# Kernel optimization log

Hardware: AMD Instinct MI355X
Metric: run time of the kernel (lower is better)

Reference implementation:

```python
import math
import jax, jax.numpy as jnp
import numpy as np

B, C, NH, H, W = 8, 512, 4, 64, 64
CH = C // 8          # qkv channels = 64
HC = CH // NH        # head channels = 16


def _pos_encoding(c, h, w):
    # Faithful to torch code, including the raw memory reinterpretation of
    # pos_h (h, c) -> (1, c, h, 1) and pos_w (c//2, 2w) -> (1, c, 1, w).
    ph = jnp.arange(h, dtype=jnp.float32)[:, None]            # (h, 1)
    pw = jnp.arange(w, dtype=jnp.float32)[None, :]            # (1, w)
    div = jnp.exp(jnp.arange(0, c, 2, dtype=jnp.float32) * (-(math.log(10000.0) / c)))
    pos_h = ph * div[None, :]                                  # (h, c/2)
    pos_w = pw * div[:, None]                                  # (c/2, w)
    pos_h = jnp.concatenate([jnp.sin(pos_h), jnp.cos(pos_h)], axis=1)  # (h, c)
    pos_w = jnp.concatenate([jnp.sin(pos_w), jnp.cos(pos_w)], axis=1)  # (c/2, 2w)
    pos_h = pos_h.reshape(1, c, h, 1)   # raw view, as in torch
    pos_w = pos_w.reshape(1, c, 1, w)   # raw view, as in torch
    return pos_h + pos_w                # (1, c, h, w)


def _conv1x1(x, w, b):
    return jnp.einsum('bchw,oc->bohw', x, w) + b[None, :, None, None]


def setup_inputs() -> dict:
    key = jax.random.key(0)
    ks = jax.random.split(key, 6)
    s = 0.02
    return {
        'x':  jax.random.normal(ks[0], (B, C, H, W), dtype=jnp.float32),
        'wq': jax.random.normal(ks[1], (CH, C), dtype=jnp.float32) * s,
        'bq': jnp.zeros((CH,), dtype=jnp.float32),
        'wk': jax.random.normal(ks[2], (CH, C), dtype=jnp.float32) * s,
        'bk': jnp.zeros((CH,), dtype=jnp.float32),
        'wv': jax.random.normal(ks[3], (CH, C), dtype=jnp.float32) * s,
        'bv': jnp.zeros((CH,), dtype=jnp.float32),
        'wo': jax.random.normal(ks[4], (C, CH), dtype=jnp.float32) * s,
        'bo': jnp.zeros((C,), dtype=jnp.float32),
        'gamma': jnp.full((1,), 0.5, dtype=jnp.float32),  # nonzero to exercise whole graph
    }


def reference(x, wq, bq, wk, bk, wv, bv, wo, bo, gamma):
    b, c, h, w = x.shape
    nh, hc = NH, HC
    x = x + _pos_encoding(c, h, w)

    q = _conv1x1(x, wq, bq).reshape(b, nh, hc, h, w)
    k = _conv1x1(x, wk, bk).reshape(b, nh, hc, h, w)
    v = _conv1x1(x, wv, bv).reshape(b, nh, hc, h, w)

    # column (H) and row (W) views
    q_H = q.transpose(0, 1, 4, 2, 3).reshape(b * nh * w, hc, h).transpose(0, 2, 1)  # (bnw, h, hc)
    q_W = q.transpose(0, 1, 3, 2, 4).reshape(b * nh * h, hc, w).transpose(0, 2, 1)  # (bnh, w, hc)
    k_H = k.transpose(0, 1, 4, 2, 3).reshape(b * nh * w, hc, h)
    k_W = k.transpose(0, 1, 3, 2, 4).reshape(b * nh * h, hc, w)
    v_H = v.transpose(0, 1, 4, 2, 3).reshape(b * nh * w, hc, h)
    v_W = v.transpose(0, 1, 3, 2, 4).reshape(b * nh * h, hc, w)

    inf_mask = jnp.where(jnp.eye(h, dtype=bool), -jnp.inf, 0.0).astype(x.dtype)  # (h, h)
    energy_H = (jnp.matmul(q_H, k_H) + inf_mask[None]).reshape(b, nh, w, h, h).transpose(0, 2, 1, 3, 4)  # (b,w,nh,h,h)
    energy_W = jnp.matmul(q_W, k_W).reshape(b, nh, h, w, w).transpose(0, 2, 1, 3, 4)                     # (b,h,nh,w,w)

    conc = jax.nn.softmax(jnp.concatenate([energy_H, energy_W], axis=4), axis=4)  # (b,w,nh,h,h+w)

    att_H = conc[..., :h].transpose(0, 2, 1, 3, 4).reshape(b * nh * w, h, h)
    # NOTE: faithful to torch: (b,h,nh,w,w) is flattened in (b,h,nh) order
    att_W = conc[..., h:h + w].reshape(b * nh * h, w, w)

    out_H = jnp.matmul(v_H, att_H.transpose(0, 2, 1))
    out_H = out_H.reshape(b, nh, w, hc, h).transpose(0, 3, 4, 1, 2).reshape(b, nh * hc, h, w)
    out_W = jnp.matmul(v_W, att_W.transpose(0, 2, 1))
    out_W = out_W.reshape(b, nh, h, hc, w).transpose(0, 3, 1, 4, 2).reshape(b, nh * hc, h, w)

    out = _conv1x1(out_H + out_W, wo, bo)
    return gamma * out + x
```

## Files before the change

### kernel.cpp

```cpp
#include <hip/hip_runtime.h>
#include <math.h>


typedef unsigned int u32;
typedef unsigned short u16;
typedef __attribute__((ext_vector_type(8))) short short8;
typedef __attribute__((ext_vector_type(4))) float f32x4;

__device__ __forceinline__ u16 f2bf(float v) {
    u32 u = __float_as_uint(v);
    u32 r = (u + 0x7FFFu + ((u >> 16) & 1u)) >> 16;
    return (u16)r;
}

__device__ __forceinline__ float bf2f(u16 v) {
    return __uint_as_float(((u32)v) << 16);
}

__device__ __forceinline__ void gll16(const void* g, void* l) {
    __builtin_amdgcn_global_load_lds(
        (const __attribute__((address_space(1))) u32*)g,
        (__attribute__((address_space(3))) u32*)l, 16, 0, 0);
}

__global__ __launch_bounds__(64) void pos_kernel(float* __restrict__ PH,
                                                 float* __restrict__ PW) {
    const float r = 0.03597789207798663f;
    int c = blockIdx.x;
    int t = threadIdx.x;
    int i = c >> 3;
    int j = ((c & 7) << 6) | t;
    float ph;
    if (j < 256) ph = sinf((float)i * expf(-(float)j * r));
    else         ph = cosf((float)i * expf(-(float)(j - 256) * r));
    PH[c * 64 + t] = ph;
    int tt = c >> 1;
    float dv = expf(-(float)tt * r);
    PW[c * 64 + t] = (c & 1) ? cosf((float)t * dv) : sinf((float)t * dv);
}

__global__ __launch_bounds__(256) void wconv_kernel(
    const float* __restrict__ wq, const float* __restrict__ wk,
    const float* __restrict__ wv, const float* __restrict__ wo,
    u16* __restrict__ WT, u16* __restrict__ WOb) {
    int i = blockIdx.x * 256 + threadIdx.x;
    if (i < 98304) {
        float v;
        if (i < 32768)      v = wq[i];
        else if (i < 65536) v = wk[i - 32768];
        else                v = wv[i - 65536];
        WT[i] = f2bf(v);
    } else {
        WOb[i - 98304] = f2bf(wo[i - 98304]);
    }
}

__global__ __launch_bounds__(256) void wpos_kernel(
    const float* __restrict__ wq, const float* __restrict__ wk,
    const float* __restrict__ wv,
    const float* __restrict__ PH, const float* __restrict__ PW,
    float* __restrict__ WPH3, float* __restrict__ WPW3) {
    int gid = blockIdx.x * 256 + threadIdx.x;
    int h = gid & 63;
    int m = (gid >> 6) & 63;
    int t = gid >> 12;
    int mg = t >> 1, tbl = t & 1;
    const float* W = (mg == 0) ? wq : (mg == 1) ? wk : wv;
    const float* P = tbl ? PW : PH;
    const float* wr = W + m * 512;
    float s = 0.f;
#pragma unroll 8
    for (int c = 0; c < 512; ++c) s += wr[c] * P[c * 64 + h];
    (tbl ? WPW3 : WPH3)[(mg * 64 + m) * 64 + h] = s;
}

__global__ __launch_bounds__(256) void qkvx_kernel(
    const float* __restrict__ x, const u16* __restrict__ WT,
    const float* __restrict__ bq, const float* __restrict__ bk,
    const float* __restrict__ bv,
    const float* __restrict__ WPH3, const float* __restrict__ WPW3,
    u16* __restrict__ Qc, u16* __restrict__ Kc, u16* __restrict__ Vc) {
    __shared__ u16 Wb[192 * 64];
    __shared__ u16 Bb[64 * 64];
    int L  = blockIdx.x;
    int b  = L & 7;
    int pt = L >> 3;
    int tid  = threadIdx.x;
    int w    = tid >> 6;
    int lane = tid & 63;
    int ln15 = lane & 15, quad = lane >> 4;
    int wm = w >> 1;
    int wp = w & 1;

    f32x4 acc[6][2];
#pragma unroll
    for (int i = 0; i < 6; ++i)
#pragma unroll
        for (int pf = 0; pf < 2; ++pf)
            acc[i][pf] = (f32x4){0.f, 0.f, 0.f, 0.f};

    const float* xb = x + (size_t)b * 2097152 + pt * 64;

    for (int kc = 0; kc < 512; kc += 64) {
        __syncthreads();
#pragma unroll
        for (int it = 0; it < 6; ++it) {
            int idx = tid + it * 256;
            int r = idx >> 3, s = idx & 7;
            gll16(WT + r * 512 + kc + ((s ^ (r & 7)) * 8), &Wb[idx * 8]);
        }
#pragma unroll
        for (int j = 0; j < 2; ++j) {
            int cc = w + j * 4;
            const float* xp = xb + (size_t)(kc + cc * 8) * 4096 + lane;
            float v[8];
#pragma unroll
            for (int i = 0; i < 8; ++i) v[i] = xp[(size_t)i * 4096];
            short8 pk;
#pragma unroll
            for (int i = 0; i < 8; ++i) pk[i] = (short)f2bf(v[i]);
            *(short8*)&Bb[lane * 64 + ((cc ^ (lane & 7)) * 8)] = pk;
        }
        __syncthreads();
#pragma unroll
        for (int ks = 0; ks < 2; ++ks) {
            int cs = ks * 4 + quad;
            short8 bf[2];
#pragma unroll
            for (int pf = 0; pf < 2; ++pf) {
                int brow = wp * 32 + pf * 16 + ln15;
                bf[pf] = *(const short8*)&Bb[brow * 64 + ((cs ^ (brow & 7)) * 8)];
            }
#pragma unroll
            for (int i = 0; i < 6; ++i) {
                int arow = (wm * 6 + i) * 16 + ln15;
                short8 af = *(const short8*)&Wb[arow * 64 + ((cs ^ (arow & 7)) * 8)];
#pragma unroll
                for (int pf = 0; pf < 2; ++pf)
                    acc[i][pf] = __builtin_amdgcn_mfma_f32_16x16x32_bf16(
                        af, bf[pf], acc[i][pf], 0, 0, 0);
            }
        }
    }

#pragma unroll
    for (int i = 0; i < 6; ++i) {
        int mf = wm * 6 + i;
        int mg = mf >> 2, nm = mf & 3;
        const float* bias = (mg == 0) ? bq : (mg == 1) ? bk : bv;
        u16* T = (mg == 0) ? Qc : (mg == 1) ? Kc : Vc;
#pragma unroll
        for (int pf = 0; pf < 2; ++pf) {
            int wc = wp * 32 + pf * 16 + ln15;
            float vals[4];
#pragma unroll
            for (int reg = 0; reg < 4; ++reg) {
                int m2 = nm * 16 + quad * 4 + reg;
                vals[reg] = acc[i][pf][reg] + bias[m2]
                          + WPH3[(mg * 64 + m2) * 64 + pt]
                          + WPW3[(mg * 64 + m2) * 64 + wc];
            }
            ushort4 pk;
            pk.x = f2bf(vals[0]);
            pk.y = f2bf(vals[1]);
            pk.z = f2bf(vals[2]);
            pk.w = f2bf(vals[3]);
            *(ushort4*)&T[(((size_t)(b * 4 + nm) * 64 + pt) * 64 + wc) * 16
                          + quad * 4] = pk;
        }
    }
}

__global__ __launch_bounds__(256, 4) void attn_kernel(
    const u16* __restrict__ Qc, const u16* __restrict__ Kc,
    const u16* __restrict__ Vc,
    u16* __restrict__ OHc, u16* __restrict__ OWc) {
    __shared__ u16 U[11008];
    u16* A_lds  = U;
    u16* B_lds  = U + 2560;
    u16* P_lds  = U;
    u16* VH_lds = U + 8704;
    u16* VW_lds = U + 9856;

    int b = blockIdx.x, n = blockIdx.y, a = blockIdx.z;
    int tid  = threadIdx.x;
    int w    = tid >> 6;
    int lane = tid & 63;
    int ln15 = lane & 15, quad = lane >> 4;
    int nv = a >> 4;
    int hv = ((a & 15) << 2) | n;

    const size_t cb = (((size_t)b * 4 + n) * 64 + a) * 1024;

    {
        int t = tid & 127;
        const short8 z8 = {0, 0, 0, 0, 0, 0, 0, 0};
        if (tid < 128) {
            int h = t >> 1, half = t & 1;
            size_t hb = (((size_t)b * 4 + n) * 64 + h) * 1024 + a * 16 + half * 8;
            short8 vA = *(const short8*)(Qc + hb);
            *(short8*)&A_lds[h * 40 + half * 8] = vA;
            short8 vK = *(const short8*)(Kc + hb);
            *(short8*)&B_lds[h * 48 + half * 8] = vK;
            *(short8*)&B_lds[h * 48 + 16 + half * 8] = z8;
            short8 vV = *(const short8*)(Vc + hb);
#pragma unroll
            for (int j = 0; j < 8; ++j)
                VH_lds[(half * 8 + j) * 72 + h] = (u16)vV[j];
        } else {
            short8 vA = *(const short8*)(Qc + cb + t * 8);
            *(short8*)&A_lds[(t >> 1) * 40 + 16 + (t & 1) * 8] = vA;
            short8 vK = *(const short8*)(Kc + cb + t * 8);
            *(short8*)&B_lds[(64 + (t >> 1)) * 48 + 16 + (t & 1) * 8] = vK;
            *(short8*)&B_lds[(64 + (t >> 1)) * 48 + (t & 1) * 8] = z8;
            size_t wb2 = (((size_t)b * 4 + nv) * 64 + hv) * 1024 + t * 8;
            short8 vV = *(const short8*)(Vc + wb2);
#pragma unroll
            for (int j = 0; j < 8; ++j)
                VW_lds[((t & 1) * 8 + j) * 72 + (t >> 1)] = (u16)vV[j];
        }
    }
    __syncthreads();

    const f32x4 zf = {0.f, 0.f, 0.f, 0.f};
    short8 af = *(const short8*)&A_lds[(w * 16 + ln15) * 40 + quad * 8];
    f32x4 acc[8];
#pragma unroll
    for (int nt = 0; nt < 8; ++nt) {
        short8 bf = *(const short8*)&B_lds[(nt * 16 + ln15) * 48 + quad * 8];
        acc[nt] = __builtin_amdgcn_mfma_f32_16x16x32_bf16(af, bf, zf, 0, 0, 0);
    }

#pragma unroll
    for (int nt = 0; nt < 4; ++nt)
#pragma unroll
        for (int r = 0; r < 4; ++r)
            if (nt * 16 + ln15 == w * 16 + quad * 4 + r) acc[nt][r] = -1e30f;

    float inv[4];
#pragma unroll
    for (int r = 0; r < 4; ++r) {
        float mrow = acc[0][r];
#pragma unroll
        for (int nt = 1; nt < 8; ++nt) mrow = fmaxf(mrow, acc[nt][r]);
        mrow = fmaxf(mrow, __shfl_xor(mrow, 1, 64));
        mrow = fmaxf(mrow, __shfl_xor(mrow, 2, 64));
        mrow = fmaxf(mrow, __shfl_xor(mrow, 4, 64));
        mrow = fmaxf(mrow, __shfl_xor(mrow, 8, 64));
        float s = 0.f;
#pragma unroll
        for (int nt = 0; nt < 8; ++nt) {
            float e = __expf(acc[nt][r] - mrow);
            acc[nt][r] = e;
            s += e;
        }
        s += __shfl_xor(s, 1, 64);
        s += __shfl_xor(s, 2, 64);
        s += __shfl_xor(s, 4, 64);
        s += __shfl_xor(s, 8, 64);
        inv[r] = 1.0f / s;
    }
    __syncthreads();
#pragma unroll
    for (int nt = 0; nt < 8; ++nt)
#pragma unroll
        for (int r = 0; r < 4; ++r)
            P_lds[(w * 16 + quad * 4 + r) * 136 + nt * 16 + ln15] =
                f2bf(acc[nt][r] * inv[r]);
    __syncthreads();

    int prow = (w * 16 + ln15) * 136;
    short8 a0 = *(const short8*)&P_lds[prow +       quad * 8];
    short8 a1 = *(const short8*)&P_lds[prow + 32  + quad * 8];
    short8 a2 = *(const short8*)&P_lds[prow + 64  + quad * 8];
    short8 a3 = *(const short8*)&P_lds[prow + 96  + quad * 8];
    short8 b0 = *(const short8*)&VH_lds[ln15 * 72 +      quad * 8];
    short8 b1 = *(const short8*)&VH_lds[ln15 * 72 + 32 + quad * 8];
    short8 c0 = *(const short8*)&VW_lds[ln15 * 72 +      quad * 8];
    short8 c1 = *(const short8*)&VW_lds[ln15 * 72 + 32 + quad * 8];
    f32x4 oH = __builtin_amdgcn_mfma_f32_16x16x32_bf16(a0, b0, zf, 0, 0, 0);
    oH = __builtin_amdgcn_mfma_f32_16x16x32_bf16(a1, b1, oH, 0, 0, 0);
    f32x4 oW = __builtin_amdgcn_mfma_f32_16x16x32_bf16(a2, c0, zf, 0, 0, 0);
    oW = __builtin_amdgcn_mfma_f32_16x16x32_bf16(a3, c1, oW, 0, 0, 0);

    __syncthreads();
    u16* eph = U;
    u16* epw = U + 16 * 68;
#pragma unroll
    for (int r = 0; r < 4; ++r) {
        eph[(quad * 4 + r) * 68 + ln15 * 4 + w]   = f2bf(oH[r]);
        epw[(w * 16 + quad * 4 + r) * 20 + ln15]  = f2bf(oW[r]);
    }
    __syncthreads();
    {
        int t = tid;
        ushort4 vh = *(const ushort4*)&eph[(t >> 4) * 68 + (t & 15) * 4];
        ushort4 vw = *(const ushort4*)&epw[(t >> 2) * 20 + (t & 3) * 4];
        size_t cbase = (((size_t)b * 4 + n) * 64 + a) * 1024;
        *(ushort4*)&OHc[cbase + t * 4] = vh;
        *(ushort4*)&OWc[cbase + t * 4] = vw;
    }
}

__global__ __launch_bounds__(256) void sconv_kernel(
    const u16* __restrict__ OHc, const u16* __restrict__ OWc,
    u16* __restrict__ Sb) {
    int b = blockIdx.x;
    int h = blockIdx.y;
    int t  = threadIdx.x;
    int wp = t >> 2;
    int cq = t & 3;

    const u16* ohp = OHc + ((((size_t)b * 4 + (h & 3)) * 64 + wp) * 1024
                            + (h >> 2) * 64 + cq * 16);
    short8 oh0 = *(const short8*)ohp;
    short8 oh1 = *(const short8*)(ohp + 8);

    const u16* owb = OWc + (((size_t)b * 4 + (wp & 3)) * 64) * 1024 + h * 16 + cq * 4;
    ushort4 owv[4];
#pragma unroll
    for (int nvi = 0; nvi < 4; ++nvi)
        owv[nvi] = *(const ushort4*)(owb + (size_t)((nvi << 4) | (wp >> 2)) * 1024);

    u16 res[16];
#pragma unroll
    for (int j = 0; j < 16; ++j) {
        u16 ohv = (j < 8) ? (u16)oh0[j] : (u16)oh1[j - 8];
        const ushort4& q = owv[j & 3];
        u16 owu = (j >> 2) == 0 ? q.x : (j >> 2) == 1 ? q.y : (j >> 2) == 2 ? q.z : q.w;
        res[j] = f2bf(bf2f(ohv) + bf2f(owu));
    }
    u16* dst = Sb + (((size_t)b * 4096 + h * 64 + wp) * 64 + cq * 16);
    *(short8*)dst       = *(short8*)&res[0];
    *(short8*)(dst + 8) = *(short8*)&res[8];
}

__global__ __launch_bounds__(256, 4) void finalm_kernel(
    const u16* __restrict__ Sb, const u16* __restrict__ WOb,
    const float* __restrict__ bo, const float* __restrict__ gamma,
    const float* __restrict__ x, const float* __restrict__ PH,
    const float* __restrict__ PW, float* __restrict__ out) {
    __shared__ u16 Ab[64 * 64];
    __shared__ u16 Bb[128 * 64];
    int pt = blockIdx.x;
    int mc = blockIdx.y;
    int b  = blockIdx.z;
    int tid  = threadIdx.x;
    int w    = tid >> 6;
    int lane = tid & 63;
    int ln15 = lane & 15, quad = lane >> 4;
    int p0 = pt * 128, m0 = mc * 64;

    float4 xv[4][2];
#pragma unroll
    for (int mf = 0; mf < 4; ++mf) {
        int m = m0 + mf * 16 + ln15;
#pragma unroll
        for (int pf = 0; pf < 2; ++pf) {
            int pb = p0 + w * 32 + pf * 16 + quad * 4;
            xv[mf][pf] = *(const float4*)&x[((size_t)(b * 512 + m)) * 4096 + pb];
        }
    }

    const u16* Ag = WOb + m0 * 64;
    const u16* Sg = Sb + ((size_t)b * 4096 + p0) * 64;

#pragma unroll
    for (int it = 0; it < 2; ++it) {
        int idx = tid + it * 256;
        int r = idx >> 3, s = idx & 7;
        gll16(Ag + r * 64 + ((s ^ (r & 7)) * 8), &Ab[idx * 8]);
    }
#pragma unroll
    for (int it = 0; it < 4; ++it) {
        int idx = tid + it * 256;
        int r = idx >> 3, s = idx & 7;
        gll16(Sg + r * 64 + ((s ^ (r & 7)) * 8), &Bb[idx * 8]);
    }
    __syncthreads();

    const f32x4 zf = {0.f, 0.f, 0.f, 0.f};
    f32x4 acc[4][2];
#pragma unroll
    for (int mf = 0; mf < 4; ++mf)
#pragma unroll
        for (int pf = 0; pf < 2; ++pf)
            acc[mf][pf] = zf;
#pragma unroll
    for (int ks = 0; ks < 2; ++ks) {
        int cs = ks * 4 + quad;
        short8 af[2], bf[4];
#pragma unroll
        for (int pf = 0; pf < 2; ++pf) {
            int row = w * 32 + pf * 16 + ln15;
            af[pf] = *(const short8*)&Bb[row * 64 + ((cs ^ (row & 7)) * 8)];
        }
#pragma unroll
        for (int mf = 0; mf < 4; ++mf) {
            int row = mf * 16 + ln15;
            bf[mf] = *(const short8*)&Ab[row * 64 + ((cs ^ (row & 7)) * 8)];
        }
#pragma unroll
        for (int mf = 0; mf < 4; ++mf)
#pragma unroll
            for (int pf = 0; pf < 2; ++pf)
                acc[mf][pf] = __builtin_amdgcn_mfma_f32_16x16x32_bf16(
                    af[pf], bf[mf], acc[mf][pf], 0, 0, 0);
    }

    float g = gamma[0];
    int h = pt * 2 + (w >> 1);
    int plb = (w & 1) * 32;
#pragma unroll
    for (int mf = 0; mf < 4; ++mf) {
        int m = m0 + mf * 16 + ln15;
        float bm = bo[m];
        float ph = PH[m * 64 + h];
#pragma unroll
        for (int pf = 0; pf < 2; ++pf) {
            int pb = p0 + w * 32 + pf * 16 + quad * 4;
            size_t o = ((size_t)(b * 512 + m)) * 4096 + pb;
            float4 pwv = *(const float4*)&PW[m * 64 + plb + pf * 16 + quad * 4];
            float4 res;
            res.x = g * (acc[mf][pf][0] + bm) + xv[mf][pf].x + ph + pwv.x;
            res.y = g * (acc[mf][pf][1] + bm) + xv[mf][pf].y + ph + pwv.y;
            res.z = g * (acc[mf][pf][2] + bm) + xv[mf][pf].z + ph + pwv.z;
            res.w = g * (acc[mf][pf][3] + bm) + xv[mf][pf].w + ph + pwv.w;
            *(float4*)&out[o] = res;
        }
    }
}

extern "C" void kernel_launch(void* const* d_in, const int* in_sizes, int n_in,
                              void* d_out, int out_size, void* d_ws, size_t ws_size,
                              hipStream_t stream) {
    const float* x     = (const float*)d_in[0];
    const float* wq    = (const float*)d_in[1];
    const float* bq    = (const float*)d_in[2];
    const float* wk    = (const float*)d_in[3];
    const float* bk    = (const float*)d_in[4];
    const float* wv    = (const float*)d_in[5];
    const float* bv    = (const float*)d_in[6];
    const float* wo    = (const float*)d_in[7];
    const float* bo    = (const float*)d_in[8];
    const float* gamma = (const float*)d_in[9];
    float* out = (float*)d_out;
    float* ws  = (float*)d_ws;

    float* PH   = ws;
    float* PW   = PH + 32768;
    float* WPH3 = PW + 32768;
    float* WPW3 = WPH3 + 12288;
    u16*   WT   = (u16*)(WPW3 + 12288);
    u16*   WOb  = WT + 98304;
    u16*   Qc   = WOb + 32768;
    u16*   Kc   = Qc + 2097152;
    u16*   Vc   = Kc + 2097152;
    u16*   OHc  = Vc + 2097152;
    u16*   OWc  = OHc + 2097152;
    u16*   Sbb  = OWc + 2097152;

    pos_kernel<<<dim3(512), dim3(64), 0, stream>>>(PH, PW);
    wconv_kernel<<<dim3(512), dim3(256), 0, stream>>>(wq, wk, wv, wo, WT, WOb);
    wpos_kernel<<<dim3(96), dim3(256), 0, stream>>>(wq, wk, wv, PH, PW, WPH3, WPW3);
    qkvx_kernel<<<dim3(512), dim3(256), 0, stream>>>(
        x, WT, bq, bk, bv, WPH3, WPW3, Qc, Kc, Vc);
    attn_kernel<<<dim3(8, 4, 64), dim3(256), 0, stream>>>(
        Qc, Kc, Vc, OHc, OWc);
    sconv_kernel<<<dim3(8, 64), dim3(256), 0, stream>>>(OHc, OWc, Sbb);
    finalm_kernel<<<dim3(32, 8, 8), dim3(256), 0, stream>>>(
        Sbb, WOb, bo, gamma, x, PH, PW, out);
}
```

Baseline: 197.5 us.

## Pre-swizzle QKV weights into MFMA fragment order and drop LDS staging

The weight conversion kernel now writes the bf16 QKV weights in a fragment-major layout, so each lane can load its MFMA A operand directly from global memory with one 16-byte load. The QKV projection kernel no longer stages weights and x tiles through shared memory and no longer needs the two barriers per k-chunk. Each wave loads and converts its own x fragments straight from global memory. This removes LDS traffic and synchronisation, but each wave now re-reads x and weights that were shared before, and the loads are not prefetched ahead of use.

```diff
diff --git a/kernel.cpp b/kernel.cpp
--- a/kernel.cpp
+++ b/kernel.cpp
@@ -42,14 +42,18 @@
 __global__ __launch_bounds__(256) void wconv_kernel(
     const float* __restrict__ wq, const float* __restrict__ wk,
     const float* __restrict__ wv, const float* __restrict__ wo,
-    u16* __restrict__ WT, u16* __restrict__ WOb) {
+    u16* __restrict__ WTf, u16* __restrict__ WOb) {
     int i = blockIdx.x * 256 + threadIdx.x;
     if (i < 98304) {
         float v;
         if (i < 32768)      v = wq[i];
         else if (i < 65536) v = wk[i - 32768];
         else                v = wv[i - 65536];
-        WT[i] = f2bf(v);
+        int r = i >> 9;
+        int c = i & 511;
+        int st = c >> 6, ks = (c >> 5) & 1, qd = (c >> 3) & 3, e = c & 7;
+        int o = (((st * 2 + ks) * 12 + (r >> 4)) * 64 + (qd * 16 + (r & 15))) * 8 + e;
+        WTf[o] = f2bf(v);
     } else {
         WOb[i - 98304] = f2bf(wo[i - 98304]);
     }
@@ -75,13 +79,11 @@
 }
 
 __global__ __launch_bounds__(256) void qkvx_kernel(
-    const float* __restrict__ x, const u16* __restrict__ WT,
+    const float* __restrict__ x, const u16* __restrict__ WTf,
     const float* __restrict__ bq, const float* __restrict__ bk,
     const float* __restrict__ bv,
     const float* __restrict__ WPH3, const float* __restrict__ WPW3,
     u16* __restrict__ Qc, u16* __restrict__ Kc, u16* __restrict__ Vc) {
-    __shared__ u16 Wb[192 * 64];
-    __shared__ u16 Bb[64 * 64];
     int L  = blockIdx.x;
     int b  = L & 7;
     int pt = L >> 3;
@@ -99,46 +101,34 @@
         for (int pf = 0; pf < 2; ++pf)
             acc[i][pf] = (f32x4){0.f, 0.f, 0.f, 0.f};
 
-    const float* xb = x + (size_t)b * 2097152 + pt * 64;
-
-    for (int kc = 0; kc < 512; kc += 64) {
-        __syncthreads();
-#pragma unroll
-        for (int it = 0; it < 6; ++it) {
-            int idx = tid + it * 256;
-            int r = idx >> 3, s = idx & 7;
-            gll16(WT + r * 512 + kc + ((s ^ (r & 7)) * 8), &Wb[idx * 8]);
-        }
-#pragma unroll
-        for (int j = 0; j < 2; ++j) {
-            int cc = w + j * 4;
-            const float* xp = xb + (size_t)(kc + cc * 8) * 4096 + lane;
-            float v[8];
-#pragma unroll
-            for (int i = 0; i < 8; ++i) v[i] = xp[(size_t)i * 4096];
-            short8 pk;
-#pragma unroll
-            for (int i = 0; i < 8; ++i) pk[i] = (short)f2bf(v[i]);
-            *(short8*)&Bb[lane * 64 + ((cc ^ (lane & 7)) * 8)] = pk;
-        }
-        __syncthreads();
+    const u16* baseW = WTf + (size_t)(wm * 6) * 512 + lane * 8;
+    const float* xbase = x + (size_t)b * 2097152
+                       + (size_t)(quad * 8) * 4096
+                       + pt * 64 + wp * 32 + ln15;
+
+    for (int st = 0; st < 8; ++st) {
 #pragma unroll
         for (int ks = 0; ks < 2; ++ks) {
-            int cs = ks * 4 + quad;
-            short8 bf[2];
+            const float* xk = xbase + (size_t)(st * 64 + ks * 32) * 4096;
+            short8 bfr[2];
 #pragma unroll
             for (int pf = 0; pf < 2; ++pf) {
-                int brow = wp * 32 + pf * 16 + ln15;
-                bf[pf] = *(const short8*)&Bb[brow * 64 + ((cs ^ (brow & 7)) * 8)];
+                float v[8];
+#pragma unroll
+                for (int e = 0; e < 8; ++e)
+                    v[e] = xk[(size_t)e * 4096 + pf * 16];
+#pragma unroll
+                for (int e = 0; e < 8; ++e)
+                    bfr[pf][e] = (short)f2bf(v[e]);
             }
+            const u16* ap = baseW + (size_t)((st * 2 + ks) * 12) * 512;
 #pragma unroll
             for (int i = 0; i < 6; ++i) {
-                int arow = (wm * 6 + i) * 16 + ln15;
-                short8 af = *(const short8*)&Wb[arow * 64 + ((cs ^ (arow & 7)) * 8)];
-#pragma unroll
-                for (int pf = 0; pf < 2; ++pf)
-                    acc[i][pf] = __builtin_amdgcn_mfma_f32_16x16x32_bf16(
-                        af, bf[pf], acc[i][pf], 0, 0, 0);
+                short8 af = *(const short8*)(ap + i * 512);
+                acc[i][0] = __builtin_amdgcn_mfma_f32_16x16x32_bf16(
+                    af, bfr[0], acc[i][0], 0, 0, 0);
+                acc[i][1] = __builtin_amdgcn_mfma_f32_16x16x32_bf16(
+                    af, bfr[1], acc[i][1], 0, 0, 0);
             }
         }
     }
@@ -451,8 +441,8 @@
     float* PW   = PH + 32768;
     float* WPH3 = PW + 32768;
     float* WPW3 = WPH3 + 12288;
-    u16*   WT   = (u16*)(WPW3 + 12288);
-    u16*   WOb  = WT + 98304;
+    u16*   WTf  = (u16*)(WPW3 + 12288);
+    u16*   WOb  = WTf + 98304;
     u16*   Qc   = WOb + 32768;
     u16*   Kc   = Qc + 2097152;
     u16*   Vc   = Kc + 2097152;
@@ -461,10 +451,10 @@
     u16*   Sbb  = OWc + 2097152;
 
     pos_kernel<<<dim3(512), dim3(64), 0, stream>>>(PH, PW);
-    wconv_kernel<<<dim3(512), dim3(256), 0, stream>>>(wq, wk, wv, wo, WT, WOb);
+    wconv_kernel<<<dim3(512), dim3(256), 0, stream>>>(wq, wk, wv, wo, WTf, WOb);
     wpos_kernel<<<dim3(96), dim3(256), 0, stream>>>(wq, wk, wv, PH, PW, WPH3, WPW3);
     qkvx_kernel<<<dim3(512), dim3(256), 0, stream>>>(
-        x, WT, bq, bk, bv, WPH3, WPW3, Qc, Kc, Vc);
+        x, WTf, bq, bk, bv, WPH3, WPW3, Qc, Kc, Vc);
     attn_kernel<<<dim3(8, 4, 64), dim3(256), 0, stream>>>(
         Qc, Kc, Vc, OHc, OWc);
     sconv_kernel<<<dim3(8, 64), dim3(256), 0, stream>>>(OHc, OWc, Sbb);
```

Result: slower. 205.9 us (+4.2%).
